# Performance work log

Measured on AMD Instinct MI355X. Metric: run time of the kernel, lower is better.

Reference implementation:

```python
import jax, jax.numpy as jnp
import numpy as np

WS = (2, 7, 7)      # window size
SS = (1, 3, 3)      # shift size
NH = 8              # num heads
DIM = 256
N = WS[0] * WS[1] * WS[2]   # 98 tokens per window
EPS = 1e-5


def _ln(x, w, b):
    m = jnp.mean(x, -1, keepdims=True)
    v = jnp.mean((x - m) ** 2, -1, keepdims=True)
    return (x - m) / jnp.sqrt(v + EPS) * w + b


def _rel_index():
    coords = np.stack(np.meshgrid(np.arange(WS[0]), np.arange(WS[1]), np.arange(WS[2]), indexing='ij'))
    cf = coords.reshape(3, -1)
    rc = (cf[:, :, None] - cf[:, None, :]).transpose(1, 2, 0).astype(np.int64)
    rc[..., 0] += WS[0] - 1
    rc[..., 1] += WS[1] - 1
    rc[..., 2] += WS[2] - 1
    rc[..., 0] *= (2 * WS[1] - 1) * (2 * WS[2] - 1)
    rc[..., 1] *= 2 * WS[2] - 1
    return rc.sum(-1).astype(np.int32)  # [N, N]


def _attn_mask(Dp, Hp, Wp):
    img = np.zeros((1, Dp, Hp, Wp, 1), np.float32)
    cnt = 0
    def sl(ws, ss):
        return (slice(0, -ws), slice(-ws, -ss), slice(-ss, None))
    for d in sl(WS[0], SS[0]):
        for h in sl(WS[1], SS[1]):
            for w in sl(WS[2], SS[2]):
                img[:, d, h, w, :] = cnt
                cnt += 1
    mw = img.reshape(1, Dp // WS[0], WS[0], Hp // WS[1], WS[1], Wp // WS[2], WS[2], 1)
    mw = mw.transpose(0, 1, 3, 5, 2, 4, 6, 7).reshape(-1, N)
    am = mw[:, None, :] - mw[:, :, None]
    return np.where(am != 0, np.float32(-100.0), np.float32(0.0)).astype(np.float32)  # [nW, N, N]


def setup_inputs() -> dict:
    key = jax.random.key(0)
    ks = jax.random.split(key, 6)
    B, D, H, W, C = 2, 16, 56, 56, DIM
    hid = 4 * C
    return {
        'x': jax.random.normal(ks[0], (B, D, H, W, C), jnp.float32),
        'mask_matrix': jnp.asarray(_attn_mask(D, H, W)),
        'rel_index': jnp.asarray(_rel_index()),
        'rel_bias_table': 0.02 * jax.random.normal(ks[1], ((2 * WS[0] - 1) * (2 * WS[1] - 1) * (2 * WS[2] - 1), NH), jnp.float32),
        'norm1_w': jnp.ones((C,), jnp.float32), 'norm1_b': jnp.zeros((C,), jnp.float32),
        'qkv_w': 0.02 * jax.random.normal(ks[2], (3 * C, C), jnp.float32), 'qkv_b': jnp.zeros((3 * C,), jnp.float32),
        'proj_w': 0.02 * jax.random.normal(ks[3], (C, C), jnp.float32), 'proj_b': jnp.zeros((C,), jnp.float32),
        'norm2_w': jnp.ones((C,), jnp.float32), 'norm2_b': jnp.zeros((C,), jnp.float32),
        'fc1_w': 0.02 * jax.random.normal(ks[4], (hid, C), jnp.float32), 'fc1_b': jnp.zeros((hid,), jnp.float32),
        'fc2_w': 0.02 * jax.random.normal(ks[5], (C, hid), jnp.float32), 'fc2_b': jnp.zeros((C,), jnp.float32),
    }


def _forward(x, mask_matrix, rel_index, rel_bias_table, norm1_w, norm1_b, qkv_w, qkv_b,
             proj_w, proj_b, norm2_w, norm2_b, fc1_w, fc1_b, fc2_w, fc2_b):
    B, D, H, W, C = x.shape
    nh, hd = NH, C // NH
    scale = hd ** -0.5
    nd, nhw, nww = D // WS[0], H // WS[1], W // WS[2]

    # --- part 1: norm -> shift -> window attention -> unshift ---
    h = _ln(x, norm1_w, norm1_b)
    h = jnp.roll(h, (-SS[0], -SS[1], -SS[2]), axis=(1, 2, 3))
    # window partition -> [B_, N, C]
    h = h.reshape(B, nd, WS[0], nhw, WS[1], nww, WS[2], C)
    h = h.transpose(0, 1, 3, 5, 2, 4, 6, 7).reshape(-1, N, C)
    B_ = h.shape[0]

    qkv = (h @ qkv_w.T + qkv_b).reshape(B_, N, 3, nh, hd).transpose(2, 0, 3, 1, 4)
    q, k, v = qkv[0], qkv[1], qkv[2]   # [B_, nh, N, hd]
    attn = jnp.einsum('bhnd,bhmd->bhnm', q * scale, k)
    bias = rel_bias_table[rel_index.reshape(-1)].reshape(N, N, nh).transpose(2, 0, 1)
    attn = attn + bias[None]
    nW = mask_matrix.shape[0]
    attn = attn.reshape(B_ // nW, nW, nh, N, N) + mask_matrix[None, :, None]
    attn = jax.nn.softmax(attn.reshape(B_, nh, N, N), axis=-1)
    o = jnp.einsum('bhnm,bhmd->bhnd', attn, v).transpose(0, 2, 1, 3).reshape(B_, N, C)
    o = o @ proj_w.T + proj_b
    # window reverse -> [B, D, H, W, C]
    o = o.reshape(B, nd, nhw, nww, WS[0], WS[1], WS[2], C)
    o = o.transpose(0, 1, 4, 2, 5, 3, 6, 7).reshape(B, D, H, W, C)
    o = jnp.roll(o, SS, axis=(1, 2, 3))

    x = x + o
    # --- part 2: MLP ---
    h2 = _ln(x, norm2_w, norm2_b)
    h2 = jax.nn.gelu(h2 @ fc1_w.T + fc1_b, approximate=False)
    return x + (h2 @ fc2_w.T + fc2_b)


def reference(x, mask_matrix, rel_index, rel_bias_table, norm1_w, norm1_b, qkv_w, qkv_b,
              proj_w, proj_b, norm2_w, norm2_b, fc1_w, fc1_b, fc2_w, fc2_b):
    return _forward(x, mask_matrix, rel_index, rel_bias_table, norm1_w, norm1_b, qkv_w, qkv_b,
                    proj_w, proj_b, norm2_w, norm2_b, fc1_w, fc1_b, fc2_w, fc2_b)
```

## Files before the change

kernel.cpp:

```cpp
#include <hip/hip_runtime.h>
#include <hip/hip_bf16.h>

typedef __attribute__((ext_vector_type(8))) short bf16x8;
typedef __attribute__((ext_vector_type(4))) float f32x4;

__device__ __forceinline__ unsigned short f2bf(float f){
  __hip_bfloat16 h = __float2bfloat16(f);
  return *reinterpret_cast<unsigned short*>(&h);
}

__device__ __forceinline__ float gelu_fast(float x){
  float z = -1.5957691216057308f * (x + 0.044715f * x*x*x);
  return x * __builtin_amdgcn_rcpf(1.f + __expf(z));
}

#define GLDS16(gptr, lptr) \
  __builtin_amdgcn_global_load_lds((const __attribute__((address_space(1))) unsigned int*)(gptr), \
                                   (__attribute__((address_space(3))) unsigned int*)(lptr), 16, 0, 0)

__global__ void prepk(const float* __restrict__ qkvw, unsigned short* __restrict__ wq,
                      const int* __restrict__ ri, const float* __restrict__ tbl,
                      const float* __restrict__ mask, unsigned short* __restrict__ combo){
  int blk = blockIdx.x;
  if (blk < 768){
    int i = blk*256 + threadIdx.x;
    wq[i] = f2bf(qkvw[i]);
    return;
  }
  int g = (blk - 768)*256 + threadIdx.x;
  if (g >= 802816) return;
  int r = g & 3;
  int t = g >> 2;
  int lane = t & 63; t >>= 6;
  int nt = t % 7; t /= 7;
  int mt = t % 7; t /= 7;
  int p = t >> 3, h = t & 7;
  int gi = mt*16 + (lane >> 4)*4 + r; if (gi > 97) gi = 97;
  int j  = nt*16 + (lane & 15);
  float v;
  if (j < 98){
    int wrep = ((p&4)?448:0) + ((p&2)?56:0) + ((p&1)?7:0);
    v = tbl[ri[gi*98 + j]*8 + h] + mask[(size_t)wrep*9604 + gi*98 + j];
  } else {
    v = -30000.f;
  }
  combo[g] = f2bf(v);
}

__global__ void cvt2k(const float* __restrict__ s1, int n1, const float* __restrict__ s2, int n2,
                      unsigned short* __restrict__ d){
  int i = blockIdx.x*256 + threadIdx.x;
  if (i < n1) d[i] = f2bf(s1[i]);
  else if (i < n1 + n2) d[i] = f2bf(s2[i - n1]);
}

__global__ void cvtk(const float* __restrict__ s, unsigned short* __restrict__ d, int n){
  int i = blockIdx.x*256 + threadIdx.x;
  if (i < n) d[i] = f2bf(s[i]);
}

__launch_bounds__(256)
__global__ void lnk(const float* __restrict__ xin, const float* __restrict__ gw, const float* __restrict__ gb,
                    unsigned short* __restrict__ hout, int mode)
{
  int wid = threadIdx.x >> 6, lane = threadIdx.x & 63;
  int tok = blockIdx.x*4 + wid;
  int src;
  if (mode == 0){
    int w = tok / 98, n = tok % 98;
    int b = w >> 9, rr = w & 511;
    int di = rr >> 6, hi = (rr >> 3) & 7, wi = rr & 7;
    int d2 = n / 49, n2 = n % 49, h2 = n2 / 7, w2 = n2 % 7;
    int sd = (di*2 + d2 + 1) & 15;
    int sh = hi*7 + h2 + 3; if (sh >= 56) sh -= 56;
    int sw = wi*7 + w2 + 3; if (sw >= 56) sw -= 56;
    src = ((b*16 + sd)*56 + sh)*56 + sw;
  } else {
    src = tok;
  }
  float4 v = *(const float4*)(xin + (size_t)src*256 + lane*4);
  float s  = v.x + v.y + v.z + v.w;
  float s2 = v.x*v.x + v.y*v.y + v.z*v.z + v.w*v.w;
  #pragma unroll
  for (int off = 1; off < 64; off <<= 1){
    s  += __shfl_xor(s, off);
    s2 += __shfl_xor(s2, off);
  }
  float mean = s * (1.f/256.f);
  float var  = s2 * (1.f/256.f) - mean*mean;
  float rstd = rsqrtf(var + 1e-5f);
  int c = lane*4;
  float4 wv = *(const float4*)(gw + c);
  float4 bv = *(const float4*)(gb + c);
  unsigned int p0 = (unsigned int)f2bf((v.x-mean)*rstd*wv.x + bv.x)
                  | ((unsigned int)f2bf((v.y-mean)*rstd*wv.y + bv.y) << 16);
  unsigned int p1 = (unsigned int)f2bf((v.z-mean)*rstd*wv.z + bv.z)
                  | ((unsigned int)f2bf((v.w-mean)*rstd*wv.w + bv.w) << 16);
  uint2 pk; pk.x = p0; pk.y = p1;
  *(uint2*)(hout + (size_t)tok*256 + c) = pk;
}

template<int EPI>
__launch_bounds__(256, 4)
__global__ void gemmk(const unsigned short* __restrict__ A, const unsigned short* __restrict__ Bw,
                      const float* __restrict__ bias, int K, int nbx,
                      unsigned short* __restrict__ outb, const float* __restrict__ xres,
                      float* __restrict__ outf, int moff)
{
  __shared__ unsigned short As[2][4096];
  __shared__ unsigned short Bs[2][4096];
  int tid = threadIdx.x;
  int wid = tid >> 6, lane = tid & 63, l16 = lane & 15, lk = lane >> 4;
  int wm = wid >> 1, wn = wid & 1;
  int cpx = gridDim.x >> 3;
  int swb = (blockIdx.x & 7)*cpx + (blockIdx.x >> 3);
  int mblk = swb / nbx, nblk = swb % nbx;
  const unsigned short* Ab = A  + (size_t)mblk*128*K;
  const unsigned short* Bb = Bw + (size_t)nblk*128*K;
  int rA = tid >> 2;
  int rB = ((rA & 15) << 2) + ((rA >> 4) & 3);
  int kcA = (((tid & 3) ^ ((tid >> 3) & 3)))*8;
  int sx = (l16 >> 1) & 3;

#define STAGE(bufi, kss) do { \
    GLDS16(Ab + (size_t)rA*K      + (kss) + kcA, &As[bufi][wid*512]); \
    GLDS16(Ab + (size_t)(rA+64)*K + (kss) + kcA, &As[bufi][2048 + wid*512]); \
    GLDS16(Bb + (size_t)rB*K      + (kss) + kcA, &Bs[bufi][wid*512]); \
    GLDS16(Bb + (size_t)(rB+64)*K + (kss) + kcA, &Bs[bufi][2048 + wid*512]); \
  } while(0)

  f32x4 acc[4][4];
  #pragma unroll
  for (int i = 0; i < 4; i++)
    #pragma unroll
    for (int j = 0; j < 4; j++)
      acc[i][j] = (f32x4){0.f,0.f,0.f,0.f};

  STAGE(0, 0);
  int cur = 0;
  for (int ks = 0; ks < K; ks += 32){
    if (ks + 32 < K){
      STAGE(cur ^ 1, ks + 32);
      asm volatile("s_waitcnt vmcnt(4)" ::: "memory");
    } else {
      asm volatile("s_waitcnt vmcnt(0)" ::: "memory");
    }
    __builtin_amdgcn_s_barrier();
    __builtin_amdgcn_sched_barrier(0);
    bf16x8 af[4], bfr[4];
    #pragma unroll
    for (int mi = 0; mi < 4; mi++) af[mi]  = *(const bf16x8*)&As[cur][(wm*64 + mi*16 + l16)*32 + (lk ^ sx)*8];
    #pragma unroll
    for (int ni = 0; ni < 4; ni++) bfr[ni] = *(const bf16x8*)&Bs[cur][(wn*64 + ni*16 + l16)*32 + (lk ^ sx)*8];
    #pragma unroll
    for (int mi = 0; mi < 4; mi++)
      #pragma unroll
      for (int ni = 0; ni < 4; ni++)
        acc[mi][ni] = __builtin_amdgcn_mfma_f32_16x16x32_bf16(af[mi], bfr[ni], acc[mi][ni], 0, 0, 0);
    __builtin_amdgcn_sched_barrier(0);
    __builtin_amdgcn_s_barrier();
    cur ^= 1;
  }
#undef STAGE

  int rowb = mblk*128 + wm*64;
  int colb = nblk*128 + wn*64;
  int c4 = colb + 4*l16;
  float4 bv = *(const float4*)(bias + c4);
  #pragma unroll
  for (int mi = 0; mi < 4; mi++){
    #pragma unroll
    for (int r = 0; r < 4; r++){
      int row = rowb + mi*16 + lk*4 + r;
      float v0 = acc[mi][0][r] + bv.x;
      float v1 = acc[mi][1][r] + bv.y;
      float v2 = acc[mi][2][r] + bv.z;
      float v3 = acc[mi][3][r] + bv.w;
      if constexpr (EPI == 0){
        if (colb < 256){
          const float sc = 0.17677669529663687f;
          v0 *= sc; v1 *= sc; v2 *= sc; v3 *= sc;
        }
        uint2 pk;
        pk.x = (unsigned int)f2bf(v0) | ((unsigned int)f2bf(v1) << 16);
        pk.y = (unsigned int)f2bf(v2) | ((unsigned int)f2bf(v3) << 16);
        *(uint2*)(outb + (size_t)row*768 + c4) = pk;
      } else if constexpr (EPI == 1){
        int w = row / 98, n = row % 98;
        int b = w >> 9, rr = w & 511;
        int di = rr >> 6, hi = (rr >> 3) & 7, wi = rr & 7;
        int d2 = n / 49, n2 = n % 49, h2 = n2 / 7, w2 = n2 % 7;
        int sd = (di*2 + d2 + 1) & 15;
        int sh = hi*7 + h2 + 3; if (sh >= 56) sh -= 56;
        int sw = wi*7 + w2 + 3; if (sw >= 56) sw -= 56;
        size_t tnat = (((size_t)b*16 + sd)*56 + sh)*56 + sw;
        float4 xr = *(const float4*)(xres + tnat*256 + c4);
        float4 ov;
        ov.x = xr.x + v0; ov.y = xr.y + v1; ov.z = xr.z + v2; ov.w = xr.w + v3;
        *(float4*)(outf + tnat*256 + c4) = ov;
      } else if constexpr (EPI == 2){
        float g0 = gelu_fast(v0);
        float g1 = gelu_fast(v1);
        float g2 = gelu_fast(v2);
        float g3 = gelu_fast(v3);
        uint2 pk;
        pk.x = (unsigned int)f2bf(g0) | ((unsigned int)f2bf(g1) << 16);
        pk.y = (unsigned int)f2bf(g2) | ((unsigned int)f2bf(g3) << 16);
        *(uint2*)(outb + (size_t)row*1024 + c4) = pk;
      } else {
        float* p = outf + (size_t)(moff + row)*256 + c4;
        float4 cu = *(const float4*)p;
        cu.x += v0; cu.y += v1; cu.z += v2; cu.w += v3;
        *(float4*)p = cu;
      }
    }
  }
}

__launch_bounds__(256)
__global__ void attnk(const unsigned short* __restrict__ qkv, const unsigned short* __restrict__ comboX,
                      unsigned short* __restrict__ obuf)
{
  __shared__ unsigned short P[4][16*136];
  int tid = threadIdx.x, wid = tid >> 6, lane = tid & 63, l16 = lane & 15, lk = lane >> 4;
  int cpx = gridDim.x >> 3;
  int swb = (blockIdx.x & 7)*cpx + (blockIdx.x >> 3);
  int task = swb*4 + wid;
  int w = task >> 3, h = task & 7;
  int rr = w & 511;
  int pat = (((rr>>6)==7)?4:0) | ((((rr>>3)&7)==7)?2:0) | (((rr&7)==7)?1:0);
  const unsigned short* cb = comboX + (size_t)(pat*8 + h)*12544;
  const unsigned short* base = qkv + (size_t)w*98*768 + h*32;

  bf16x8 kfr[7];
  #pragma unroll
  for (int nt = 0; nt < 7; nt++){
    int kc = nt*16 + l16; if (kc > 97) kc = 97;
    kfr[nt] = *(const bf16x8*)(base + (size_t)kc*768 + 256 + lk*8);
  }
  bf16x8 v0[4], v1[4];
  #pragma unroll
  for (int kcc = 0; kcc < 4; kcc++){
    #pragma unroll
    for (int j = 0; j < 8; j++){
      int k = kcc*32 + lk*8 + j; if (k > 97) k = 97;
      unsigned int u = *(const unsigned int*)(base + (size_t)k*768 + 512 + 2*l16);
      v0[kcc][j] = (short)(u & 0xffff);
      v1[kcc][j] = (short)(u >> 16);
    }
  }
  bf16x8 vones;
  #pragma unroll
  for (int j = 0; j < 8; j++) vones[j] = (short)0x3F80;

  unsigned short* Pw = &P[wid][0];
  { int rp = lane >> 2, cc = 112 + (lane & 3)*4;
    *(uint2*)&Pw[rp*136 + cc] = make_uint2(0u, 0u); }

  for (int mt = 0; mt < 7; mt++){
    int qrow = mt*16 + l16; if (qrow > 97) qrow = 97;
    bf16x8 qa = *(const bf16x8*)(base + (size_t)qrow*768 + lk*8);

    const unsigned short* cm = cb + mt*1792;
    f32x4 s[7];
    #pragma unroll
    for (int nt = 0; nt < 7; nt++){
      uint2 c2 = *(const uint2*)(cm + (nt*64 + lane)*4);
      f32x4 ci;
      ci[0] = __uint_as_float(c2.x << 16);
      ci[1] = __uint_as_float(c2.x & 0xffff0000u);
      ci[2] = __uint_as_float(c2.y << 16);
      ci[3] = __uint_as_float(c2.y & 0xffff0000u);
      s[nt] = __builtin_amdgcn_mfma_f32_16x16x32_bf16(qa, kfr[nt], ci, 0, 0, 0);
    }

    float mx[4] = {-3e38f,-3e38f,-3e38f,-3e38f};
    #pragma unroll
    for (int nt = 0; nt < 7; nt++){
      mx[0] = fmaxf(mx[0], s[nt][0]); mx[1] = fmaxf(mx[1], s[nt][1]);
      mx[2] = fmaxf(mx[2], s[nt][2]); mx[3] = fmaxf(mx[3], s[nt][3]);
    }
    float mxa = fmaxf(fmaxf(mx[0], mx[1]), fmaxf(mx[2], mx[3]));
    #pragma unroll
    for (int off = 1; off < 64; off <<= 1) mxa = fmaxf(mxa, __shfl_xor(mxa, off));

    #pragma unroll
    for (int r = 0; r < 4; r++)
      #pragma unroll
      for (int nt = 0; nt < 7; nt++)
        Pw[(lk*4 + r)*136 + nt*16 + l16] = f2bf(__expf(s[nt][r] - mxa));

    f32x4 o0 = (f32x4){0.f,0.f,0.f,0.f}, o1 = (f32x4){0.f,0.f,0.f,0.f};
    f32x4 os = (f32x4){0.f,0.f,0.f,0.f};
    #pragma unroll
    for (int kcc = 0; kcc < 4; kcc++){
      bf16x8 pa = *(const bf16x8*)&Pw[l16*136 + kcc*32 + lk*8];
      __builtin_amdgcn_s_setprio(1);
      o0 = __builtin_amdgcn_mfma_f32_16x16x32_bf16(pa, v0[kcc], o0, 0, 0, 0);
      o1 = __builtin_amdgcn_mfma_f32_16x16x32_bf16(pa, v1[kcc], o1, 0, 0, 0);
      os = __builtin_amdgcn_mfma_f32_16x16x32_bf16(pa, vones,   os, 0, 0, 0);
      __builtin_amdgcn_s_setprio(0);
    }
    #pragma unroll
    for (int r = 0; r < 4; r++){
      int n = mt*16 + lk*4 + r;
      if (n < 98){
        float inv = __builtin_amdgcn_rcpf(os[r]);
        unsigned int pk = (unsigned int)f2bf(o0[r]*inv) | ((unsigned int)f2bf(o1[r]*inv) << 16);
        *(unsigned int*)(obuf + ((size_t)w*98 + n)*256 + h*32 + 2*l16) = pk;
      }
    }
  }
}

extern "C" void kernel_launch(void* const* d_in, const int* in_sizes, int n_in,
                              void* d_out, int out_size, void* d_ws, size_t ws_size,
                              hipStream_t stream)
{
  const float* x     = (const float*)d_in[0];
  const float* maskm = (const float*)d_in[1];
  const int*   ri    = (const int*)d_in[2];
  const float* tbl   = (const float*)d_in[3];
  const float* n1w   = (const float*)d_in[4];
  const float* n1b   = (const float*)d_in[5];
  const float* qkvw  = (const float*)d_in[6];
  const float* qkvbv = (const float*)d_in[7];
  const float* projw = (const float*)d_in[8];
  const float* projb = (const float*)d_in[9];
  const float* n2w   = (const float*)d_in[10];
  const float* n2b   = (const float*)d_in[11];
  const float* fc1w  = (const float*)d_in[12];
  const float* fc1b  = (const float*)d_in[13];
  const float* fc2w  = (const float*)d_in[14];
  const float* fc2b  = (const float*)d_in[15];
  float* dout = (float*)d_out;
  char* ws = (char*)d_ws;

  unsigned short* qkvB  = (unsigned short*)(ws + 0);
  unsigned short* hb    = (unsigned short*)(ws + 154140672);
  unsigned short* wq    = (unsigned short*)(ws + 205520896);
  unsigned short* comboX= (unsigned short*)(ws + 205914112);
  unsigned short* wp = (unsigned short*)(ws + 0);
  unsigned short* w1 = (unsigned short*)(ws + 131072);
  unsigned short* w2 = (unsigned short*)(ws + 655360);
  unsigned short* h2 = (unsigned short*)(ws + 2097152);
  unsigned short* g  = (unsigned short*)(ws + 53477376);

  prepk<<<3904, 256, 0, stream>>>(qkvw, wq, ri, tbl, maskm, comboX);

  lnk<<<25088, 256, 0, stream>>>(x, n1w, n1b, hb, 0);
  gemmk<0><<<784*6, 256, 0, stream>>>(hb, wq, qkvbv, 256, 6, qkvB, nullptr, nullptr, 0);
  attnk<<<2048, 256, 0, stream>>>(qkvB, comboX, hb);
  cvtk<<<256, 256, 0, stream>>>(projw, wp, 65536);
  cvt2k<<<2048, 256, 0, stream>>>(fc1w, 262144, fc2w, 262144, w1);
  gemmk<1><<<784*2, 256, 0, stream>>>(hb, wp, projb, 256, 2, nullptr, x, dout, 0);

  lnk<<<25088, 256, 0, stream>>>(dout, n2w, n2b, h2, 1);
  for (int c = 0; c < 2; c++){
    gemmk<2><<<392*8, 256, 0, stream>>>(h2 + (size_t)c*50176*256, w1, fc1b, 256, 8, g, nullptr, nullptr, 0);
    gemmk<3><<<392*2, 256, 0, stream>>>(g, w2, fc2b, 1024, 2, nullptr, nullptr, dout, c*50176);
  }
}
```

Measured before the change: 459.6 us.

## Widen GEMM tiles to 128x256 for K=256 GEMMs with vectorized epilogues

Adds a gemmw kernel that computes 128x256 output tiles (each wave covers 64x128) for the QKV, projection and FC1 GEMMs, halving the block count. The B rows are permuted so that each lane's eight accumulator columns are contiguous, which allows 16-byte packed bf16 stores and paired float4 residual writes. The aim is more reuse of each A tile per block and fewer redundant A reads, at the cost of twice the accumulator registers and lower occupancy (launch bounds drop from 4 to 2 blocks). FC2 keeps the old 128x128 kernel, now specialised into gemmk3.

```diff
diff --git a/kernel.cpp b/kernel.cpp
--- a/kernel.cpp
+++ b/kernel.cpp
@@ -101,11 +101,137 @@
 }
 
 template<int EPI>
-__launch_bounds__(256, 4)
-__global__ void gemmk(const unsigned short* __restrict__ A, const unsigned short* __restrict__ Bw,
+__launch_bounds__(256, 2)
+__global__ void gemmw(const unsigned short* __restrict__ A, const unsigned short* __restrict__ Bw,
                       const float* __restrict__ bias, int K, int nbx,
                       unsigned short* __restrict__ outb, const float* __restrict__ xres,
-                      float* __restrict__ outf, int moff)
+                      float* __restrict__ outf)
+{
+  __shared__ unsigned short As[2][4096];
+  __shared__ unsigned short Bs[2][8192];
+  int tid = threadIdx.x;
+  int wid = tid >> 6, lane = tid & 63, l16 = lane & 15, lk = lane >> 4;
+  int wm = wid >> 1, wn = wid & 1;
+  int cpx = gridDim.x >> 3;
+  int swb = (blockIdx.x & 7)*cpx + (blockIdx.x >> 3);
+  int mblk = swb / nbx, nblk = swb % nbx;
+  const unsigned short* Ab = A  + (size_t)mblk*128*K;
+  const unsigned short* Bb = Bw + (size_t)nblk*256*K;
+  int rA = tid >> 2;
+  int rB[4];
+  #pragma unroll
+  for (int q = 0; q < 4; q++){
+    int rho = q*64 + rA;
+    rB[q] = ((rho >> 7) << 7) + ((rho & 15) << 3) + ((rho >> 4) & 7);
+  }
+  int kcA = (((tid & 3) ^ ((tid >> 3) & 3)))*8;
+  int sx = (l16 >> 1) & 3;
+
+#define STAGEW(bufi, kss) do { \
+    GLDS16(Ab + (size_t)rA*K      + (kss) + kcA, &As[bufi][wid*512]); \
+    GLDS16(Ab + (size_t)(rA+64)*K + (kss) + kcA, &As[bufi][2048 + wid*512]); \
+    GLDS16(Bb + (size_t)rB[0]*K   + (kss) + kcA, &Bs[bufi][wid*512]); \
+    GLDS16(Bb + (size_t)rB[1]*K   + (kss) + kcA, &Bs[bufi][2048 + wid*512]); \
+    GLDS16(Bb + (size_t)rB[2]*K   + (kss) + kcA, &Bs[bufi][4096 + wid*512]); \
+    GLDS16(Bb + (size_t)rB[3]*K   + (kss) + kcA, &Bs[bufi][6144 + wid*512]); \
+  } while(0)
+
+  f32x4 acc[4][8];
+  #pragma unroll
+  for (int i = 0; i < 4; i++)
+    #pragma unroll
+    for (int j = 0; j < 8; j++)
+      acc[i][j] = (f32x4){0.f,0.f,0.f,0.f};
+
+  STAGEW(0, 0);
+  int cur = 0;
+  for (int ks = 0; ks < K; ks += 32){
+    if (ks + 32 < K){
+      STAGEW(cur ^ 1, ks + 32);
+      asm volatile("s_waitcnt vmcnt(6)" ::: "memory");
+    } else {
+      asm volatile("s_waitcnt vmcnt(0)" ::: "memory");
+    }
+    __builtin_amdgcn_s_barrier();
+    __builtin_amdgcn_sched_barrier(0);
+    bf16x8 af[4], bfr[8];
+    #pragma unroll
+    for (int mi = 0; mi < 4; mi++) af[mi]  = *(const bf16x8*)&As[cur][(wm*64 + mi*16 + l16)*32 + (lk ^ sx)*8];
+    #pragma unroll
+    for (int ni = 0; ni < 8; ni++) bfr[ni] = *(const bf16x8*)&Bs[cur][(wn*128 + ni*16 + l16)*32 + (lk ^ sx)*8];
+    #pragma unroll
+    for (int mi = 0; mi < 4; mi++)
+      #pragma unroll
+      for (int ni = 0; ni < 8; ni++)
+        acc[mi][ni] = __builtin_amdgcn_mfma_f32_16x16x32_bf16(af[mi], bfr[ni], acc[mi][ni], 0, 0, 0);
+    __builtin_amdgcn_sched_barrier(0);
+    __builtin_amdgcn_s_barrier();
+    cur ^= 1;
+  }
+#undef STAGEW
+
+  int rowb = mblk*128 + wm*64;
+  int colb = nblk*256;
+  int c8 = colb + wn*128 + 8*l16;
+  float4 bva = *(const float4*)(bias + c8);
+  float4 bvb = *(const float4*)(bias + c8 + 4);
+  #pragma unroll
+  for (int mi = 0; mi < 4; mi++){
+    #pragma unroll
+    for (int r = 0; r < 4; r++){
+      int row = rowb + mi*16 + lk*4 + r;
+      float v0 = acc[mi][0][r] + bva.x;
+      float v1 = acc[mi][1][r] + bva.y;
+      float v2 = acc[mi][2][r] + bva.z;
+      float v3 = acc[mi][3][r] + bva.w;
+      float v4 = acc[mi][4][r] + bvb.x;
+      float v5 = acc[mi][5][r] + bvb.y;
+      float v6 = acc[mi][6][r] + bvb.z;
+      float v7 = acc[mi][7][r] + bvb.w;
+      if constexpr (EPI == 0){
+        if (nblk == 0){
+          const float sc = 0.17677669529663687f;
+          v0 *= sc; v1 *= sc; v2 *= sc; v3 *= sc;
+          v4 *= sc; v5 *= sc; v6 *= sc; v7 *= sc;
+        }
+        uint4 pk;
+        pk.x = (unsigned int)f2bf(v0) | ((unsigned int)f2bf(v1) << 16);
+        pk.y = (unsigned int)f2bf(v2) | ((unsigned int)f2bf(v3) << 16);
+        pk.z = (unsigned int)f2bf(v4) | ((unsigned int)f2bf(v5) << 16);
+        pk.w = (unsigned int)f2bf(v6) | ((unsigned int)f2bf(v7) << 16);
+        *(uint4*)(outb + (size_t)row*768 + c8) = pk;
+      } else if constexpr (EPI == 1){
+        int w = row / 98, n = row % 98;
+        int b = w >> 9, rr = w & 511;
+        int di = rr >> 6, hi = (rr >> 3) & 7, wi = rr & 7;
+        int d2 = n / 49, n2 = n % 49, h2 = n2 / 7, w2 = n2 % 7;
+        int sd = (di*2 + d2 + 1) & 15;
+        int sh = hi*7 + h2 + 3; if (sh >= 56) sh -= 56;
+        int sw = wi*7 + w2 + 3; if (sw >= 56) sw -= 56;
+        size_t tnat = (((size_t)b*16 + sd)*56 + sh)*56 + sw;
+        float4 xr0 = *(const float4*)(xres + tnat*256 + c8);
+        float4 xr1 = *(const float4*)(xres + tnat*256 + c8 + 4);
+        float4 oa, ob2;
+        oa.x = xr0.x + v0; oa.y = xr0.y + v1; oa.z = xr0.z + v2; oa.w = xr0.w + v3;
+        ob2.x = xr1.x + v4; ob2.y = xr1.y + v5; ob2.z = xr1.z + v6; ob2.w = xr1.w + v7;
+        *(float4*)(outf + tnat*256 + c8)     = oa;
+        *(float4*)(outf + tnat*256 + c8 + 4) = ob2;
+      } else {
+        uint4 pk;
+        pk.x = (unsigned int)f2bf(gelu_fast(v0)) | ((unsigned int)f2bf(gelu_fast(v1)) << 16);
+        pk.y = (unsigned int)f2bf(gelu_fast(v2)) | ((unsigned int)f2bf(gelu_fast(v3)) << 16);
+        pk.z = (unsigned int)f2bf(gelu_fast(v4)) | ((unsigned int)f2bf(gelu_fast(v5)) << 16);
+        pk.w = (unsigned int)f2bf(gelu_fast(v6)) | ((unsigned int)f2bf(gelu_fast(v7)) << 16);
+        *(uint4*)(outb + (size_t)row*1024 + c8) = pk;
+      }
+    }
+  }
+}
+
+__launch_bounds__(256, 4)
+__global__ void gemmk3(const unsigned short* __restrict__ A, const unsigned short* __restrict__ Bw,
+                       const float* __restrict__ bias, int K, int nbx,
+                       float* __restrict__ outf, int moff)
 {
   __shared__ unsigned short As[2][4096];
   __shared__ unsigned short Bs[2][4096];
@@ -122,7 +248,7 @@
   int kcA = (((tid & 3) ^ ((tid >> 3) & 3)))*8;
   int sx = (l16 >> 1) & 3;
 
-#define STAGE(bufi, kss) do { \
+#define STAGE3(bufi, kss) do { \
     GLDS16(Ab + (size_t)rA*K      + (kss) + kcA, &As[bufi][wid*512]); \
     GLDS16(Ab + (size_t)(rA+64)*K + (kss) + kcA, &As[bufi][2048 + wid*512]); \
     GLDS16(Bb + (size_t)rB*K      + (kss) + kcA, &Bs[bufi][wid*512]); \
@@ -136,11 +262,11 @@
     for (int j = 0; j < 4; j++)
       acc[i][j] = (f32x4){0.f,0.f,0.f,0.f};
 
-  STAGE(0, 0);
+  STAGE3(0, 0);
   int cur = 0;
   for (int ks = 0; ks < K; ks += 32){
     if (ks + 32 < K){
-      STAGE(cur ^ 1, ks + 32);
+      STAGE3(cur ^ 1, ks + 32);
       asm volatile("s_waitcnt vmcnt(4)" ::: "memory");
     } else {
       asm volatile("s_waitcnt vmcnt(0)" ::: "memory");
@@ -161,7 +287,7 @@
     __builtin_amdgcn_s_barrier();
     cur ^= 1;
   }
-#undef STAGE
+#undef STAGE3
 
   int rowb = mblk*128 + wm*64;
   int colb = nblk*128 + wn*64;
@@ -172,47 +298,13 @@
     #pragma unroll
     for (int r = 0; r < 4; r++){
       int row = rowb + mi*16 + lk*4 + r;
-      float v0 = acc[mi][0][r] + bv.x;
-      float v1 = acc[mi][1][r] + bv.y;
-      float v2 = acc[mi][2][r] + bv.z;
-      float v3 = acc[mi][3][r] + bv.w;
-      if constexpr (EPI == 0){
-        if (colb < 256){
-          const float sc = 0.17677669529663687f;
-          v0 *= sc; v1 *= sc; v2 *= sc; v3 *= sc;
-        }
-        uint2 pk;
-        pk.x = (unsigned int)f2bf(v0) | ((unsigned int)f2bf(v1) << 16);
-        pk.y = (unsigned int)f2bf(v2) | ((unsigned int)f2bf(v3) << 16);
-        *(uint2*)(outb + (size_t)row*768 + c4) = pk;
-      } else if constexpr (EPI == 1){
-        int w = row / 98, n = row % 98;
-        int b = w >> 9, rr = w & 511;
-        int di = rr >> 6, hi = (rr >> 3) & 7, wi = rr & 7;
-        int d2 = n / 49, n2 = n % 49, h2 = n2 / 7, w2 = n2 % 7;
-        int sd = (di*2 + d2 + 1) & 15;
-        int sh = hi*7 + h2 + 3; if (sh >= 56) sh -= 56;
-        int sw = wi*7 + w2 + 3; if (sw >= 56) sw -= 56;
-        size_t tnat = (((size_t)b*16 + sd)*56 + sh)*56 + sw;
-        float4 xr = *(const float4*)(xres + tnat*256 + c4);
-        float4 ov;
-        ov.x = xr.x + v0; ov.y = xr.y + v1; ov.z = xr.z + v2; ov.w = xr.w + v3;
-        *(float4*)(outf + tnat*256 + c4) = ov;
-      } else if constexpr (EPI == 2){
-        float g0 = gelu_fast(v0);
-        float g1 = gelu_fast(v1);
-        float g2 = gelu_fast(v2);
-        float g3 = gelu_fast(v3);
-        uint2 pk;
-        pk.x = (unsigned int)f2bf(g0) | ((unsigned int)f2bf(g1) << 16);
-        pk.y = (unsigned int)f2bf(g2) | ((unsigned int)f2bf(g3) << 16);
-        *(uint2*)(outb + (size_t)row*1024 + c4) = pk;
-      } else {
-        float* p = outf + (size_t)(moff + row)*256 + c4;
-        float4 cu = *(const float4*)p;
-        cu.x += v0; cu.y += v1; cu.z += v2; cu.w += v3;
-        *(float4*)p = cu;
-      }
+      float* p = outf + (size_t)(moff + row)*256 + c4;
+      float4 cu = *(const float4*)p;
+      cu.x += acc[mi][0][r] + bv.x;
+      cu.y += acc[mi][1][r] + bv.y;
+      cu.z += acc[mi][2][r] + bv.z;
+      cu.w += acc[mi][3][r] + bv.w;
+      *(float4*)p = cu;
     }
   }
 }
@@ -349,15 +441,15 @@
   prepk<<<3904, 256, 0, stream>>>(qkvw, wq, ri, tbl, maskm, comboX);
 
   lnk<<<25088, 256, 0, stream>>>(x, n1w, n1b, hb, 0);
-  gemmk<0><<<784*6, 256, 0, stream>>>(hb, wq, qkvbv, 256, 6, qkvB, nullptr, nullptr, 0);
+  gemmw<0><<<784*3, 256, 0, stream>>>(hb, wq, qkvbv, 256, 3, qkvB, nullptr, nullptr);
   attnk<<<2048, 256, 0, stream>>>(qkvB, comboX, hb);
   cvtk<<<256, 256, 0, stream>>>(projw, wp, 65536);
   cvt2k<<<2048, 256, 0, stream>>>(fc1w, 262144, fc2w, 262144, w1);
-  gemmk<1><<<784*2, 256, 0, stream>>>(hb, wp, projb, 256, 2, nullptr, x, dout, 0);
+  gemmw<1><<<784, 256, 0, stream>>>(hb, wp, projb, 256, 1, nullptr, x, dout);
 
   lnk<<<25088, 256, 0, stream>>>(dout, n2w, n2b, h2, 1);
   for (int c = 0; c < 2; c++){
-    gemmk<2><<<392*8, 256, 0, stream>>>(h2 + (size_t)c*50176*256, w1, fc1b, 256, 8, g, nullptr, nullptr, 0);
-    gemmk<3><<<392*2, 256, 0, stream>>>(g, w2, fc2b, 1024, 2, nullptr, nullptr, dout, c*50176);
-  }
-}
+    gemmw<2><<<392*4, 256, 0, stream>>>(h2 + (size_t)c*50176*256, w1, fc1b, 256, 4, g, nullptr, nullptr);
+    gemmk3<<<392*2, 256, 0, stream>>>(g, w2, fc2b, 1024, 2, dout, c*50176);
+  }
+}
```

Result: slower. 489.1 us (+6.4%).
